# Optimization experiments

Measured on AMD Instinct MI355X. Metric: run time of the kernel, lower is better.

Reference implementation:

```python
import jax, jax.numpy as jnp
import numpy as np

N = 1_000_000
Km = 16
Ks = 64
LB, RT = -1.0, 1.0  # hemi=False -> lb=(-1,-1), rt=(1,1)
TWO_PI = 2.0 * np.pi


def setup_inputs() -> dict:
    key = jax.random.key(0)
    ks = jax.random.split(key, 12)
    r = jax.random.uniform(ks[0], (N, 1), jnp.float32, -0.999, 0.999)
    z = jax.random.uniform(ks[1], (N, 1), jnp.float32, 0.0, TWO_PI)
    theta_w = jax.random.normal(ks[2], (1, Ks), jnp.float32)
    theta_h = jax.random.normal(ks[3], (1, Ks), jnp.float32)
    theta_d = jax.random.normal(ks[4], (1, Ks - 1), jnp.float32)
    W1 = jax.random.normal(ks[5], (1, 64), jnp.float32)
    b1 = jax.random.normal(ks[6], (64,), jnp.float32) * 0.1
    W2 = jax.random.normal(ks[7], (64, 64), jnp.float32) / np.float32(np.sqrt(64))
    b2 = jax.random.normal(ks[8], (64,), jnp.float32) * 0.1
    W3 = jax.random.normal(ks[9], (64, 3 * Km), jnp.float32) / np.float32(np.sqrt(64))
    b3 = jax.random.normal(ks[10], (3 * Km,), jnp.float32) * 0.1
    return dict(r=r, z=z, theta_w=theta_w, theta_h=theta_h, theta_d=theta_d,
                W1=W1, b1=b1, W2=W2, b2=b2, W3=W3, b3=b3)


def _spline(r, theta_w, theta_h, theta_d):
    # Unconditional rational-quadratic circular spline on (LB, RT).
    width = jax.nn.softmax(theta_w, axis=1) * (RT - LB)    # [1,Ks]
    height = jax.nn.softmax(theta_h, axis=1) * (RT - LB)
    zero = jnp.zeros((1, 1), width.dtype)
    x_ks = jnp.concatenate([zero, jnp.cumsum(width, axis=1)], axis=1) + LB   # [1,Ks+1]
    y_ks = jnp.concatenate([zero, jnp.cumsum(height, axis=1)], axis=1) + LB
    bnd = jnp.full((1, 1), (RT - LB) / (RT - LB), width.dtype)
    derivs = jnp.concatenate([bnd, jax.nn.softplus(theta_d) + 0.001, bnd], axis=1)  # [1,Ks+1]

    x = r[:, 0]                                             # [N]
    k = jnp.searchsorted(x_ks[0], x)                        # left side, matches torch default
    k = jnp.where(k == 0, 1, k)
    k = jnp.where(k == Ks + 1, Ks, k)
    k = k - 1
    nk = k + 1
    x_k, x_nk = x_ks[0, k], x_ks[0, nk]
    y_k, y_nk = y_ks[0, k], y_ks[0, nk]
    d_k, d_nk = derivs[0, k], derivs[0, nk]

    s_k = (y_nk - y_k) / (x_nk - x_k)
    eps = (x - x_k) / (x_nk - x_k)
    denom = s_k + (d_nk + d_k - 2.0 * s_k) * eps * (1.0 - eps)
    tx = y_k + (y_nk - y_k) * (s_k * eps ** 2 + d_k * eps * (1.0 - eps)) / denom
    dtx = s_k ** 2 * (d_nk * eps ** 2 + 2.0 * s_k * eps * (1.0 - eps) + d_k * (1.0 - eps) ** 2) / denom ** 2
    return tx[:, None], dtx


def _mobius(x, r, W1, b1, W2, b2, W3, b3):
    # Conditional Mobius transform on the circle; conditioner = 2-hidden MLP on r.
    h = jax.nn.relu(r @ W1 + b1)
    h = jax.nn.relu(h @ W2 + b2)
    theta = h @ W3 + b3                                     # [N,3Km]
    weights = jax.nn.softmax(theta[:, :Km], axis=1)         # [N,Km]
    w = theta[:, Km:].reshape(-1, Km, 2)                    # [N,Km,2]
    w = 0.99 / (1.0 + jnp.linalg.norm(w, axis=-1, keepdims=True)) * w

    def h_map(zv, w):
        # zv: [M,2] broadcast against w: [N,Km,2]
        diff = zv[:, None, :] - w
        wn2 = jnp.sum(w * w, axis=-1, keepdims=True)
        dn2 = jnp.sum(diff * diff, axis=-1, keepdims=True)
        return (1.0 - wn2) / dn2 * diff - w

    zv = jnp.concatenate([jnp.cos(x), jnp.sin(x)], axis=1)  # [N,2]
    h_z = h_map(zv, w)                                      # [N,Km,2]
    h_0 = h_map(jnp.array([[1.0, 0.0]], zv.dtype), w)
    radians = jnp.arctan2(h_z[..., 1], h_z[..., 0])
    shifts = jnp.arctan2(h_0[..., 1], h_0[..., 0])
    tx = radians - shifts
    tx = jnp.where(tx >= 0, tx, tx + TWO_PI)
    t = jnp.sum(weights * tx, axis=1, keepdims=True)        # [N,1]

    # Jacobian magnitude: dh/dz is c*(I - 2 u u^T) (scaled reflection), applied to dz/dtheta
    diff = zv[:, None, :] - w
    dn = jnp.linalg.norm(diff, axis=-1)                     # [N,Km]
    u = diff / dn[..., None]
    dz = jnp.concatenate([-jnp.sin(x), jnp.cos(x)], axis=1) # [N,2]
    c = (1.0 - jnp.sum(w * w, axis=-1)) / dn ** 2           # [N,Km]
    udz = jnp.sum(u * dz[:, None, :], axis=-1)              # [N,Km]
    dh = c[..., None] * (dz[:, None, :] - 2.0 * u * udz[..., None])  # [N,Km,2]
    dt = jnp.sum(jnp.linalg.norm(dh, axis=-1) * weights, axis=1)     # [N]
    return t, dt


def reference(r, z, theta_w, theta_h, theta_d, W1, b1, W2, b2, W3, b3):
    tr, dtr = _spline(r, theta_w, theta_h, theta_d)
    tz, dtz = _mobius(z, r, W1, b1, W2, b2, W3, b3)
    ldj = jnp.log(dtr) + jnp.log(dtz)
    return tr, tz, ldj
```

## Files before the change

### kernel.cpp

```cpp
#include <hip/hip_runtime.h>
#include <math.h>

#define KM 16
#define KS 64
#define TWO_PI_F 6.283185307179586477f

#define WS_SXK   0
#define WS_SYK   65
#define WS_SDK   130
#define WS_KNOT  195
#define WS_A     259
#define WS_B     (259 + 4225)

__device__ __forceinline__ float frcp(float x) { return __builtin_amdgcn_rcpf(x); }

__device__ __forceinline__ float fast_atan2(float y, float x) {
    const float ax = fabsf(x), ay = fabsf(y);
    const float mx = fmaxf(ax, ay), mn = fminf(ax, ay);
    const float t = mn * frcp(mx);
    const float s = t * t;
    float p = -0.01172120f;
    p = fmaf(p, s,  0.05265332f);
    p = fmaf(p, s, -0.11643287f);
    p = fmaf(p, s,  0.19354346f);
    p = fmaf(p, s, -0.33262347f);
    p = fmaf(p, s,  0.99997726f);
    p = p * t;
    p = (ay > ax) ? (1.57079632679f - p) : p;
    p = (x < 0.0f) ? (3.14159265359f - p) : p;
    p = (y < 0.0f) ? -p : p;
    return p;
}

__global__ __launch_bounds__(256)
void precompute_kernel(const float* __restrict__ theta_w,
                       const float* __restrict__ theta_h,
                       const float* __restrict__ theta_d,
                       const float* __restrict__ W1,
                       const float* __restrict__ b1,
                       const float* __restrict__ W2,
                       const float* __restrict__ b2,
                       float* __restrict__ ws)
{
    __shared__ float sW1[64], sb1[64], tjs[64];
    __shared__ int   srnk[64];
    __shared__ float sW2[64 * 64];

    const int tid = threadIdx.x;

    if (tid < 64) {
        const float w1 = W1[tid];
        const float bb = b1[tid];
        sW1[tid] = w1;
        sb1[tid] = bb;
        tjs[tid] = (w1 != 0.0f) ? (-bb / w1) : INFINITY;
    }
    {
        const float4* __restrict__ W2v = (const float4*)W2;
        float4* __restrict__ sW2v = (float4*)sW2;
        for (int t2 = tid; t2 < 1024; t2 += 256) sW2v[t2] = W2v[t2];
    }
    __syncthreads();

    if (tid < 64) {
        const float t = tjs[tid];
        int rk = 0;
        #pragma unroll 1
        for (int k2 = 0; k2 < 64; k2++) {
            const float tk = tjs[k2];
            rk += (tk < t || (tk == t && k2 < tid)) ? 1 : 0;
        }
        srnk[tid] = rk;
    }
    __syncthreads();

    if (blockIdx.x == 0 && tid < 64) {
        ws[WS_KNOT + srnk[tid]] = tjs[tid];

        float vw = theta_w[tid];
        float vh = theta_h[tid];
        float mw = vw, mh = vh;
        #pragma unroll
        for (int off = 32; off > 0; off >>= 1) {
            mw = fmaxf(mw, __shfl_xor(mw, off));
            mh = fmaxf(mh, __shfl_xor(mh, off));
        }
        const float ew = expf(vw - mw);
        const float eh = expf(vh - mh);
        float sumw = ew, sumh = eh;
        #pragma unroll
        for (int off = 32; off > 0; off >>= 1) {
            sumw += __shfl_xor(sumw, off);
            sumh += __shfl_xor(sumh, off);
        }
        float cw = ew / sumw * 2.0f;
        float ch = eh / sumh * 2.0f;
        #pragma unroll
        for (int off = 1; off < 64; off <<= 1) {
            const float uw = __shfl_up(cw, off);
            const float uh = __shfl_up(ch, off);
            if (tid >= off) { cw += uw; ch += uh; }
        }
        ws[WS_SXK + 1 + tid] = cw - 1.0f;
        ws[WS_SYK + 1 + tid] = ch - 1.0f;
        if (tid < KS - 1) {
            const float x = theta_d[tid];
            const float sp = (x > 20.0f) ? x : log1pf(expf(x));
            ws[WS_SDK + 1 + tid] = sp + 0.001f;
        }
        if (tid == 0) {
            ws[WS_SXK] = -1.0f;
            ws[WS_SYK] = -1.0f;
            ws[WS_SDK] = 1.0f;
            ws[WS_SDK + KS] = 1.0f;
        }
    }

    const int p = blockIdx.x * 256 + tid;
    if (p < 65 * 64) {
        const int v = p >> 6;
        const int i = p & 63;
        float cA = 0.0f;
        float cB = b2[i];
        #pragma unroll 1
        for (int j = 0; j < 64; j++) {
            const float w1 = sW1[j];
            const float bb = sb1[j];
            const float w2 = sW2[j * 64 + i];
            if (w1 > 0.0f) {
                if (srnk[j] < v)  { cA = fmaf(w1, w2, cA); cB = fmaf(bb, w2, cB); }
            } else if (w1 < 0.0f) {
                if (srnk[j] >= v) { cA = fmaf(w1, w2, cA); cB = fmaf(bb, w2, cB); }
            } else {
                cB = fmaf(fmaxf(bb, 0.0f), w2, cB);
            }
        }
        ws[WS_A + v * 65 + i] = cA;
        ws[WS_B + v * 65 + i] = cB;
    }
}

__global__ __launch_bounds__(256)
void mobius_spline_kernel(const float* __restrict__ r_in,
                          const float* __restrict__ z_in,
                          const float* __restrict__ W3,
                          const float* __restrict__ b3,
                          const float* __restrict__ ws,
                          float* __restrict__ out,
                          int n)
{
    __shared__ float sxk[KS + 1], syk[KS + 1], sdk[KS + 1];
    __shared__ float sknot[KS];
    __shared__ float sA[65 * 65], sB[65 * 65];

    const int tid = threadIdx.x;

    for (int t2 = tid; t2 < 65; t2 += 256) {
        sxk[t2] = ws[WS_SXK + t2];
        syk[t2] = ws[WS_SYK + t2];
        sdk[t2] = ws[WS_SDK + t2];
    }
    for (int t2 = tid; t2 < 64; t2 += 256) sknot[t2] = ws[WS_KNOT + t2];
    for (int t2 = tid; t2 < 4225; t2 += 256) {
        sA[t2] = ws[WS_A + t2];
        sB[t2] = ws[WS_B + t2];
    }
    __syncthreads();

    const int idx = blockIdx.x * 256 + tid;
    if (idx >= n) return;

    const float rv = r_in[idx];
    const float zz = z_in[idx];

    int lo = 0, hi = KS + 1;
    while (lo < hi) {
        const int mid = (lo + hi) >> 1;
        if (sxk[mid] < rv) lo = mid + 1; else hi = mid;
    }
    int k = lo;
    k = (k == 0) ? 1 : k;
    k = (k == KS + 1) ? KS : k;
    k -= 1;
    const float x_k = sxk[k], x_nk = sxk[k + 1];
    const float y_k = syk[k], y_nk = syk[k + 1];
    const float d_k = sdk[k], d_nk = sdk[k + 1];
    const float rdx = frcp(x_nk - x_k);
    const float dy  = y_nk - y_k;
    const float s_k = dy * rdx;
    const float eps = (rv - x_k) * rdx;
    const float ome = 1.0f - eps;
    const float den = s_k + (d_nk + d_k - 2.0f * s_k) * eps * ome;
    const float rden = frcp(den);
    const float tr  = fmaf(dy * (s_k * eps * eps + d_k * eps * ome), rden, y_k);
    const float dtr = s_k * s_k * (d_nk * eps * eps + 2.0f * s_k * eps * ome + d_k * ome * ome)
                      * rden * rden;

    int lo2 = 0, hi2 = KS;
    while (lo2 < hi2) {
        const int mid = (lo2 + hi2) >> 1;
        if (sknot[mid] < rv) lo2 = mid + 1; else hi2 = mid;
    }
    const int abase = lo2 * 65;

    float th[16], wx[16], wy[16];
    #pragma unroll
    for (int q = 0; q < 16; q++) {
        th[q] = b3[q];
        wx[q] = b3[16 + 2 * q];
        wy[q] = b3[17 + 2 * q];
    }

    #pragma unroll 4
    for (int i = 0; i < 64; i++) {
        const float hv = fmaxf(fmaf(rv, sA[abase + i], sB[abase + i]), 0.0f);
        const float* __restrict__ w3r = &W3[i * 48];
        #pragma unroll
        for (int q = 0; q < 16; q++) {
            th[q] = fmaf(hv, w3r[q],          th[q]);
            wx[q] = fmaf(hv, w3r[16 + 2 * q], wx[q]);
            wy[q] = fmaf(hv, w3r[17 + 2 * q], wy[q]);
        }
    }

    float mx = th[0];
    #pragma unroll
    for (int q = 1; q < 16; q++) mx = fmaxf(mx, th[q]);

    float cz, sz;
    __sincosf(zz, &sz, &cz);

    float wsum = 0.0f, tsum = 0.0f, dsum = 0.0f;

    #pragma unroll
    for (int q = 0; q < 16; q++) {
        const float rwx = wx[q], rwy = wy[q];
        const float nrm = __builtin_amdgcn_sqrtf(rwx * rwx + rwy * rwy);
        const float scl = 0.99f * frcp(1.0f + nrm);
        const float wxx = scl * rwx, wyy = scl * rwy;
        const float wn2 = wxx * wxx + wyy * wyy;
        const float omw = 1.0f - wn2;
        const float dzx = cz - wxx, dzy = sz - wyy;
        const float dn2z = dzx * dzx + dzy * dzy;
        const float cf = omw * frcp(dn2z);
        const float hzx = cf * dzx - wxx;
        const float hzy = cf * dzy - wyy;
        const float d0x = 1.0f - wxx, d0y = -wyy;
        const float dn20 = d0x * d0x + d0y * d0y;
        const float c0 = omw * frcp(dn20);
        const float h0x = c0 * d0x - wxx;
        const float h0y = c0 * d0y - wyy;
        const float cross = hzy * h0x - hzx * h0y;
        const float dotp  = hzx * h0x + hzy * h0y;
        float tx = fast_atan2(cross, dotp);
        tx = (tx >= 0.0f) ? tx : tx + TWO_PI_F;

        const float ew = __expf(th[q] - mx);
        wsum += ew;
        tsum += ew * tx;
        dsum += ew * cf;
    }

    const float inv = frcp(wsum);
    const float tz  = tsum * inv;
    const float dtz = dsum * inv;
    const float ldj = __logf(dtr) + __logf(dtz);

    out[idx]         = tr;
    out[n + idx]     = tz;
    out[2 * n + idx] = ldj;
}

extern "C" void kernel_launch(void* const* d_in, const int* in_sizes, int n_in,
                              void* d_out, int out_size, void* d_ws, size_t ws_size,
                              hipStream_t stream) {
    const int n = in_sizes[0];
    float* ws = (float*)d_ws;

    hipLaunchKernelGGL(precompute_kernel, dim3(17), dim3(256), 0, stream,
                       (const float*)d_in[2], (const float*)d_in[3],
                       (const float*)d_in[4], (const float*)d_in[5],
                       (const float*)d_in[6], (const float*)d_in[7],
                       (const float*)d_in[8], ws);

    const int blocks = (n + 255) / 256;
    hipLaunchKernelGGL(mobius_spline_kernel, dim3(blocks), dim3(256), 0, stream,
                       (const float*)d_in[0], (const float*)d_in[1],
                       (const float*)d_in[9], (const float*)d_in[10],
                       (const float*)ws,
                       (float*)d_out, n);
}
```

Baseline: 179.3 us.

## Precompute piecewise-linear MLP output coefficients per ReLU activation region

The conditioner MLP is piecewise linear in r, so each point's region is set by the layer-1 knot interval and the sorted layer-2 ReLU roots inside it. The new precompute kernel finds those roots for all 65 intervals and precomputes affine coefficients for the 48 outputs in every sub-region. The main kernel then does two small binary searches and evaluates 48 fmas from one global row, replacing the per-point 64x48 layer-3 matmul. The cost is a larger workspace (about 1.6 MB), scattered global reads of the coefficient rows, and a fallback path that runs when the workspace is too small.

Result: faster. 167.4 us (-6.6%).

```diff
diff --git a/kernel.cpp b/kernel.cpp
--- a/kernel.cpp
+++ b/kernel.cpp
@@ -11,6 +11,9 @@
 #define WS_KNOT  195
 #define WS_A     259
 #define WS_B     (259 + 4225)
+#define WS_SROOT 8709
+#define WS_COEF  12872
+#define WS_NEED  (12872 + 4225 * 96)
 
 __device__ __forceinline__ float frcp(float x) { return __builtin_amdgcn_rcpf(x); }
 
@@ -33,35 +36,44 @@
 }
 
 __global__ __launch_bounds__(256)
-void precompute_kernel(const float* __restrict__ theta_w,
-                       const float* __restrict__ theta_h,
-                       const float* __restrict__ theta_d,
-                       const float* __restrict__ W1,
-                       const float* __restrict__ b1,
-                       const float* __restrict__ W2,
-                       const float* __restrict__ b2,
-                       float* __restrict__ ws)
+void precompute_full(const float* __restrict__ theta_w,
+                     const float* __restrict__ theta_h,
+                     const float* __restrict__ theta_d,
+                     const float* __restrict__ W1,
+                     const float* __restrict__ b1,
+                     const float* __restrict__ W2,
+                     const float* __restrict__ b2,
+                     const float* __restrict__ W3,
+                     const float* __restrict__ b3,
+                     float* __restrict__ ws)
 {
-    __shared__ float sW1[64], sb1[64], tjs[64];
+    __shared__ float sW1[64], sb1[64], tjs[64], sknotS[64];
     __shared__ int   srnk[64];
     __shared__ float sW2[64 * 64];
+    __shared__ float sW3[64 * 48];
+    __shared__ float sb3[48];
+    __shared__ float sAv[64], sBv[64], rroot[64], rsort[64], rmid[65];
 
     const int tid = threadIdx.x;
-
-    if (tid < 64) {
-        const float w1 = W1[tid];
-        const float bb = b1[tid];
-        sW1[tid] = w1;
-        sb1[tid] = bb;
-        tjs[tid] = (w1 != 0.0f) ? (-bb / w1) : INFINITY;
-    }
+    const int v = blockIdx.x;
+
+    if (tid < 64) { sW1[tid] = W1[tid]; sb1[tid] = b1[tid]; }
     {
-        const float4* __restrict__ W2v = (const float4*)W2;
-        float4* __restrict__ sW2v = (float4*)sW2;
-        for (int t2 = tid; t2 < 1024; t2 += 256) sW2v[t2] = W2v[t2];
-    }
-    __syncthreads();
-
+        const float4* __restrict__ a = (const float4*)W2;
+        float4* b = (float4*)sW2;
+        for (int t = tid; t < 1024; t += 256) b[t] = a[t];
+    }
+    {
+        const float4* __restrict__ a = (const float4*)W3;
+        float4* b = (float4*)sW3;
+        for (int t = tid; t < 768; t += 256) b[t] = a[t];
+    }
+    if (tid < 48) sb3[tid] = b3[tid];
+    __syncthreads();
+
+    if (tid < 64)
+        tjs[tid] = (sW1[tid] != 0.0f) ? (-sb1[tid] / sW1[tid]) : INFINITY;
+    __syncthreads();
     if (tid < 64) {
         const float t = tjs[tid];
         int rk = 0;
@@ -71,12 +83,289 @@
             rk += (tk < t || (tk == t && k2 < tid)) ? 1 : 0;
         }
         srnk[tid] = rk;
+        sknotS[rk] = t;
+    }
+    __syncthreads();
+
+    if (tid < 64) {
+        const int i = tid;
+        float cA = 0.0f, cB = b2[i];
+        #pragma unroll 1
+        for (int j = 0; j < 64; j++) {
+            const float w1 = sW1[j];
+            const float bb = sb1[j];
+            const float w2 = sW2[j * 64 + i];
+            if (w1 > 0.0f) {
+                if (srnk[j] < v)  { cA = fmaf(w1, w2, cA); cB = fmaf(bb, w2, cB); }
+            } else if (w1 < 0.0f) {
+                if (srnk[j] >= v) { cA = fmaf(w1, w2, cA); cB = fmaf(bb, w2, cB); }
+            } else {
+                cB = fmaf(fmaxf(bb, 0.0f), w2, cB);
+            }
+        }
+        sAv[i] = cA; sBv[i] = cB;
+    }
+    __syncthreads();
+
+    if (tid < 64)
+        rroot[tid] = (sAv[tid] != 0.0f) ? (-sBv[tid] / sAv[tid]) : INFINITY;
+    __syncthreads();
+    if (tid < 64) {
+        const float t = rroot[tid];
+        int rk = 0;
+        #pragma unroll 1
+        for (int k2 = 0; k2 < 64; k2++) {
+            const float tk = rroot[k2];
+            rk += (tk < t || (tk == t && k2 < tid)) ? 1 : 0;
+        }
+        rsort[rk] = t;
+        ws[WS_SROOT + v * 64 + rk] = t;
+    }
+    __syncthreads();
+
+    const float x_lo = (v == 0)  ? -1.0f : sknotS[v - 1];
+    const float x_hi = (v == 64) ?  1.0f : sknotS[v];
+    if (tid < 65) {
+        const int s = tid;
+        const float lo = (s == 0)  ? x_lo : fmaxf(x_lo, rsort[s - 1]);
+        const float hi = (s == 64) ? x_hi : fminf(x_hi, rsort[s]);
+        rmid[s] = 0.5f * (lo + hi);
+    }
+    __syncthreads();
+
+    for (int p = tid; p < 65 * 48; p += 256) {
+        const int s = p / 48;
+        const int o = p - 48 * s;
+        const float rm = rmid[s];
+        float a = 0.0f, b = sb3[o];
+        #pragma unroll 4
+        for (int j = 0; j < 64; j++) {
+            const float A = sAv[j], B = sBv[j];
+            const float w3 = sW3[j * 48 + o];
+            const float m = (fmaf(A, rm, B) > 0.0f) ? w3 : 0.0f;
+            a = fmaf(A, m, a);
+            b = fmaf(B, m, b);
+        }
+        float* __restrict__ row = ws + WS_COEF + (v * 65 + s) * 96;
+        row[2 * o]     = a;
+        row[2 * o + 1] = b;
+    }
+
+    if (v == 0 && tid < 64) {
+        ws[WS_KNOT + tid] = sknotS[tid];
+
+        float vw = theta_w[tid];
+        float vh = theta_h[tid];
+        float mw = vw, mh = vh;
+        #pragma unroll
+        for (int off = 32; off > 0; off >>= 1) {
+            mw = fmaxf(mw, __shfl_xor(mw, off));
+            mh = fmaxf(mh, __shfl_xor(mh, off));
+        }
+        const float ew = expf(vw - mw);
+        const float eh = expf(vh - mh);
+        float sumw = ew, sumh = eh;
+        #pragma unroll
+        for (int off = 32; off > 0; off >>= 1) {
+            sumw += __shfl_xor(sumw, off);
+            sumh += __shfl_xor(sumh, off);
+        }
+        float cw = ew / sumw * 2.0f;
+        float ch = eh / sumh * 2.0f;
+        #pragma unroll
+        for (int off = 1; off < 64; off <<= 1) {
+            const float uw = __shfl_up(cw, off);
+            const float uh = __shfl_up(ch, off);
+            if (tid >= off) { cw += uw; ch += uh; }
+        }
+        ws[WS_SXK + 1 + tid] = cw - 1.0f;
+        ws[WS_SYK + 1 + tid] = ch - 1.0f;
+        if (tid < KS - 1) {
+            const float x = theta_d[tid];
+            const float sp = (x > 20.0f) ? x : log1pf(expf(x));
+            ws[WS_SDK + 1 + tid] = sp + 0.001f;
+        }
+        if (tid == 0) {
+            ws[WS_SXK] = -1.0f;
+            ws[WS_SYK] = -1.0f;
+            ws[WS_SDK] = 1.0f;
+            ws[WS_SDK + KS] = 1.0f;
+        }
+    }
+}
+
+__global__ __launch_bounds__(256)
+void mobius_spline_kernel(const float* __restrict__ r_in,
+                          const float* __restrict__ z_in,
+                          const float* __restrict__ ws,
+                          float* __restrict__ out,
+                          int n)
+{
+    __shared__ float sxk[KS + 1], syk[KS + 1], sdk[KS + 1];
+    __shared__ float sknot[KS];
+    __shared__ float sroots[65 * 65];
+
+    const int tid = threadIdx.x;
+
+    for (int t2 = tid; t2 < 65; t2 += 256) {
+        sxk[t2] = ws[WS_SXK + t2];
+        syk[t2] = ws[WS_SYK + t2];
+        sdk[t2] = ws[WS_SDK + t2];
+    }
+    for (int t2 = tid; t2 < 64; t2 += 256) sknot[t2] = ws[WS_KNOT + t2];
+    for (int t2 = tid; t2 < 65 * 64; t2 += 256) {
+        const int v2 = t2 >> 6, m = t2 & 63;
+        sroots[v2 * 65 + m] = ws[WS_SROOT + t2];
+    }
+    __syncthreads();
+
+    const int idx = blockIdx.x * 256 + tid;
+    if (idx >= n) return;
+
+    const float rv = r_in[idx];
+    const float zz = z_in[idx];
+
+    int lo = 0, hi = KS + 1;
+    while (lo < hi) {
+        const int mid = (lo + hi) >> 1;
+        if (sxk[mid] < rv) lo = mid + 1; else hi = mid;
+    }
+    int k = lo;
+    k = (k == 0) ? 1 : k;
+    k = (k == KS + 1) ? KS : k;
+    k -= 1;
+    const float x_k = sxk[k], x_nk = sxk[k + 1];
+    const float y_k = syk[k], y_nk = syk[k + 1];
+    const float d_k = sdk[k], d_nk = sdk[k + 1];
+    const float rdx = frcp(x_nk - x_k);
+    const float dy  = y_nk - y_k;
+    const float s_k = dy * rdx;
+    const float eps = (rv - x_k) * rdx;
+    const float ome = 1.0f - eps;
+    const float den = s_k + (d_nk + d_k - 2.0f * s_k) * eps * ome;
+    const float rden = frcp(den);
+    const float tr  = fmaf(dy * (s_k * eps * eps + d_k * eps * ome), rden, y_k);
+    const float dtr = s_k * s_k * (d_nk * eps * eps + 2.0f * s_k * eps * ome + d_k * ome * ome)
+                      * rden * rden;
+
+    int lo2 = 0, hi2 = KS;
+    while (lo2 < hi2) {
+        const int mid = (lo2 + hi2) >> 1;
+        if (sknot[mid] < rv) lo2 = mid + 1; else hi2 = mid;
+    }
+    const int v = lo2;
+    const int rbase = v * 65;
+    int lo3 = 0, hi3 = 64;
+    while (lo3 < hi3) {
+        const int mid = (lo3 + hi3) >> 1;
+        if (sroots[rbase + mid] < rv) lo3 = mid + 1; else hi3 = mid;
+    }
+    const int s = lo3;
+
+    const float4* __restrict__ row4 =
+        (const float4*)(ws + WS_COEF + (size_t)(v * 65 + s) * 96);
+
+    float th[16];
+    #pragma unroll
+    for (int o8 = 0; o8 < 8; o8++) {
+        const float4 c = row4[o8];
+        th[2 * o8]     = fmaf(c.x, rv, c.y);
+        th[2 * o8 + 1] = fmaf(c.z, rv, c.w);
+    }
+    float mx = th[0];
+    #pragma unroll
+    for (int q = 1; q < 16; q++) mx = fmaxf(mx, th[q]);
+
+    float cz, sz;
+    __sincosf(zz, &sz, &cz);
+
+    float wsum = 0.0f, tsum = 0.0f, dsum = 0.0f;
+
+    #pragma unroll 4
+    for (int q = 0; q < 16; q++) {
+        const float4 c = row4[8 + q];
+        const float rwx = fmaf(c.x, rv, c.y);
+        const float rwy = fmaf(c.z, rv, c.w);
+        const float nrm = __builtin_amdgcn_sqrtf(rwx * rwx + rwy * rwy);
+        const float scl = 0.99f * frcp(1.0f + nrm);
+        const float wxx = scl * rwx, wyy = scl * rwy;
+        const float wn2 = wxx * wxx + wyy * wyy;
+        const float omw = 1.0f - wn2;
+        const float dzx = cz - wxx, dzy = sz - wyy;
+        const float dn2z = dzx * dzx + dzy * dzy;
+        const float cf = omw * frcp(dn2z);
+        const float hzx = cf * dzx - wxx;
+        const float hzy = cf * dzy - wyy;
+        const float d0x = 1.0f - wxx, d0y = -wyy;
+        const float dn20 = d0x * d0x + d0y * d0y;
+        const float c0 = omw * frcp(dn20);
+        const float h0x = c0 * d0x - wxx;
+        const float h0y = c0 * d0y - wyy;
+        const float cross = hzy * h0x - hzx * h0y;
+        const float dotp  = hzx * h0x + hzy * h0y;
+        float tx = fast_atan2(cross, dotp);
+        tx = (tx >= 0.0f) ? tx : tx + TWO_PI_F;
+
+        const float ew = __expf(th[q] - mx);
+        wsum += ew;
+        tsum += ew * tx;
+        dsum += ew * cf;
+    }
+
+    const float inv = frcp(wsum);
+    const float tz  = tsum * inv;
+    const float dtz = dsum * inv;
+    const float ldj = __logf(dtr) + __logf(dtz);
+
+    out[idx]         = tr;
+    out[n + idx]     = tz;
+    out[2 * n + idx] = ldj;
+}
+
+__global__ __launch_bounds__(256)
+void precompute_fb(const float* __restrict__ theta_w,
+                   const float* __restrict__ theta_h,
+                   const float* __restrict__ theta_d,
+                   const float* __restrict__ W1,
+                   const float* __restrict__ b1,
+                   const float* __restrict__ W2,
+                   const float* __restrict__ b2,
+                   float* __restrict__ ws)
+{
+    __shared__ float sW1[64], sb1[64], tjs[64];
+    __shared__ int   srnk[64];
+    __shared__ float sW2[64 * 64];
+
+    const int tid = threadIdx.x;
+
+    if (tid < 64) {
+        const float w1 = W1[tid];
+        const float bb = b1[tid];
+        sW1[tid] = w1;
+        sb1[tid] = bb;
+        tjs[tid] = (w1 != 0.0f) ? (-bb / w1) : INFINITY;
+    }
+    {
+        const float4* __restrict__ W2v = (const float4*)W2;
+        float4* __restrict__ sW2v = (float4*)sW2;
+        for (int t2 = tid; t2 < 1024; t2 += 256) sW2v[t2] = W2v[t2];
+    }
+    __syncthreads();
+
+    if (tid < 64) {
+        const float t = tjs[tid];
+        int rk = 0;
+        #pragma unroll 1
+        for (int k2 = 0; k2 < 64; k2++) {
+            const float tk = tjs[k2];
+            rk += (tk < t || (tk == t && k2 < tid)) ? 1 : 0;
+        }
+        srnk[tid] = rk;
     }
     __syncthreads();
 
     if (blockIdx.x == 0 && tid < 64) {
         ws[WS_KNOT + srnk[tid]] = tjs[tid];
-
         float vw = theta_w[tid];
         float vh = theta_h[tid];
         float mw = vw, mh = vh;
@@ -141,13 +430,13 @@
 }
 
 __global__ __launch_bounds__(256)
-void mobius_spline_kernel(const float* __restrict__ r_in,
-                          const float* __restrict__ z_in,
-                          const float* __restrict__ W3,
-                          const float* __restrict__ b3,
-                          const float* __restrict__ ws,
-                          float* __restrict__ out,
-                          int n)
+void mobius_spline_fb(const float* __restrict__ r_in,
+                      const float* __restrict__ z_in,
+                      const float* __restrict__ W3,
+                      const float* __restrict__ b3,
+                      const float* __restrict__ ws,
+                      float* __restrict__ out,
+                      int n)
 {
     __shared__ float sxk[KS + 1], syk[KS + 1], sdk[KS + 1];
     __shared__ float sknot[KS];
@@ -276,17 +565,27 @@
                               hipStream_t stream) {
     const int n = in_sizes[0];
     float* ws = (float*)d_ws;
-
-    hipLaunchKernelGGL(precompute_kernel, dim3(17), dim3(256), 0, stream,
-                       (const float*)d_in[2], (const float*)d_in[3],
-                       (const float*)d_in[4], (const float*)d_in[5],
-                       (const float*)d_in[6], (const float*)d_in[7],
-                       (const float*)d_in[8], ws);
-
     const int blocks = (n + 255) / 256;
-    hipLaunchKernelGGL(mobius_spline_kernel, dim3(blocks), dim3(256), 0, stream,
-                       (const float*)d_in[0], (const float*)d_in[1],
-                       (const float*)d_in[9], (const float*)d_in[10],
-                       (const float*)ws,
-                       (float*)d_out, n);
+
+    if (ws_size >= (size_t)WS_NEED * sizeof(float)) {
+        hipLaunchKernelGGL(precompute_full, dim3(65), dim3(256), 0, stream,
+                           (const float*)d_in[2], (const float*)d_in[3],
+                           (const float*)d_in[4], (const float*)d_in[5],
+                           (const float*)d_in[6], (const float*)d_in[7],
+                           (const float*)d_in[8], (const float*)d_in[9],
+                           (const float*)d_in[10], ws);
+        hipLaunchKernelGGL(mobius_spline_kernel, dim3(blocks), dim3(256), 0, stream,
+                           (const float*)d_in[0], (const float*)d_in[1],
+                           (const float*)ws, (float*)d_out, n);
+    } else {
+        hipLaunchKernelGGL(precompute_fb, dim3(17), dim3(256), 0, stream,
+                           (const float*)d_in[2], (const float*)d_in[3],
+                           (const float*)d_in[4], (const float*)d_in[5],
+                           (const float*)d_in[6], (const float*)d_in[7],
+                           (const float*)d_in[8], ws);
+        hipLaunchKernelGGL(mobius_spline_fb, dim3(blocks), dim3(256), 0, stream,
+                           (const float*)d_in[0], (const float*)d_in[1],
+                           (const float*)d_in[9], (const float*)d_in[10],
+                           (const float*)ws, (float*)d_out, n);
+    }
 }
```

## Precompute piecewise-linear layer-3 coefficients per ReLU interval and fuse via cooperative grid

Applied to the files above, without the earlier changes.

Because the input to layer 1 is the scalar r, layers 2 and 3 are piecewise-linear in r. Each of the 65 knot intervals is split again at the 64 layer-2 ReLU roots, and a 48-output affine coefficient pair is precomputed for every sub-interval. Each point then runs two binary searches and reads 96 floats instead of doing a 64x48 matmul. The precompute and main pass are fused into one cooperative persistent kernel with a grid sync, falling back to two launches. The cost is a large coefficient table (about 1.6MB) read from global or L2 per point, with scattered row accesses, and the overhead of the grid sync. Note that the else branch still uses the new layout, so if the workspace is too small the table writes would overflow.

Result: slower. 356.1 us (+98.6%).

```diff
diff --git a/kernel.cpp b/kernel.cpp
--- a/kernel.cpp
+++ b/kernel.cpp
@@ -1,5 +1,8 @@
 #include <hip/hip_runtime.h>
+#include <hip/hip_cooperative_groups.h>
 #include <math.h>
+
+namespace cg = cooperative_groups;
 
 #define KM 16
 #define KS 64
@@ -9,8 +12,9 @@
 #define WS_SYK   65
 #define WS_SDK   130
 #define WS_KNOT  195
-#define WS_A     259
-#define WS_B     (259 + 4225)
+#define WS_SROOT 8709
+#define WS_COEF  12872
+#define WS_NEED  (12872 + 4225 * 96)
 
 __device__ __forceinline__ float frcp(float x) { return __builtin_amdgcn_rcpf(x); }
 
@@ -32,50 +36,101 @@
     return p;
 }
 
-__global__ __launch_bounds__(256)
-void precompute_kernel(const float* __restrict__ theta_w,
-                       const float* __restrict__ theta_h,
-                       const float* __restrict__ theta_d,
-                       const float* __restrict__ W1,
-                       const float* __restrict__ b1,
-                       const float* __restrict__ W2,
-                       const float* __restrict__ b2,
-                       float* __restrict__ ws)
+__device__ __forceinline__ void precompute_interval(
+    int v, int tid,
+    const float* __restrict__ theta_w, const float* __restrict__ theta_h,
+    const float* __restrict__ theta_d,
+    const float* __restrict__ W1, const float* __restrict__ b1,
+    const float* __restrict__ W2, const float* __restrict__ b2,
+    const float* __restrict__ W3, const float* __restrict__ b3,
+    float* __restrict__ ws,
+    float* p_tjs, float* p_sAv, float* p_sBv, float* p_sknotS, float* p_rroot,
+    int* p_srnk, int* p_jinv)
 {
-    __shared__ float sW1[64], sb1[64], tjs[64];
-    __shared__ int   srnk[64];
-    __shared__ float sW2[64 * 64];
-
-    const int tid = threadIdx.x;
-
     if (tid < 64) {
-        const float w1 = W1[tid];
-        const float bb = b1[tid];
-        sW1[tid] = w1;
-        sb1[tid] = bb;
-        tjs[tid] = (w1 != 0.0f) ? (-bb / w1) : INFINITY;
-    }
-    {
-        const float4* __restrict__ W2v = (const float4*)W2;
-        float4* __restrict__ sW2v = (float4*)sW2;
-        for (int t2 = tid; t2 < 1024; t2 += 256) sW2v[t2] = W2v[t2];
-    }
-    __syncthreads();
-
+        const float w1 = W1[tid], bb = b1[tid];
+        p_tjs[tid] = (w1 != 0.0f) ? (-bb / w1) : INFINITY;
+    }
+    __syncthreads();
     if (tid < 64) {
-        const float t = tjs[tid];
+        const float t = p_tjs[tid];
         int rk = 0;
-        #pragma unroll 1
+        #pragma unroll 8
         for (int k2 = 0; k2 < 64; k2++) {
-            const float tk = tjs[k2];
+            const float tk = p_tjs[k2];
             rk += (tk < t || (tk == t && k2 < tid)) ? 1 : 0;
         }
-        srnk[tid] = rk;
-    }
-    __syncthreads();
-
-    if (blockIdx.x == 0 && tid < 64) {
-        ws[WS_KNOT + srnk[tid]] = tjs[tid];
+        p_srnk[tid] = rk;
+        p_sknotS[rk] = t;
+    }
+    __syncthreads();
+
+    if (tid < 64) {
+        const int i = tid;
+        float cA = 0.0f, cB = b2[i];
+        #pragma unroll 8
+        for (int j = 0; j < 64; j++) {
+            const float w1 = W1[j];
+            const float bb = b1[j];
+            const float w2 = W2[j * 64 + i];
+            if (w1 > 0.0f) {
+                if (p_srnk[j] < v)  { cA = fmaf(w1, w2, cA); cB = fmaf(bb, w2, cB); }
+            } else if (w1 < 0.0f) {
+                if (p_srnk[j] >= v) { cA = fmaf(w1, w2, cA); cB = fmaf(bb, w2, cB); }
+            } else {
+                cB = fmaf(fmaxf(bb, 0.0f), w2, cB);
+            }
+        }
+        p_sAv[i] = cA; p_sBv[i] = cB;
+    }
+    __syncthreads();
+
+    if (tid < 64)
+        p_rroot[tid] = (p_sAv[tid] != 0.0f) ? (-p_sBv[tid] / p_sAv[tid]) : INFINITY;
+    __syncthreads();
+    if (tid < 64) {
+        const float t = p_rroot[tid];
+        int rk = 0;
+        #pragma unroll 8
+        for (int k2 = 0; k2 < 64; k2++) {
+            const float tk = p_rroot[k2];
+            rk += (tk < t || (tk == t && k2 < tid)) ? 1 : 0;
+        }
+        p_jinv[rk] = tid;
+        ws[WS_SROOT + v * 64 + rk] = t;
+    }
+    __syncthreads();
+
+    if (tid < 48) {
+        const int o = tid;
+        float a = 0.0f, b = b3[o];
+        #pragma unroll 8
+        for (int j = 0; j < 64; j++) {
+            const float A = p_sAv[j], B = p_sBv[j];
+            const float w3 = W3[j * 48 + o];
+            const bool act = (A < 0.0f) || (A == 0.0f && B > 0.0f);
+            const float m = act ? w3 : 0.0f;
+            a = fmaf(A, m, a);
+            b = fmaf(B, m, b);
+        }
+        float* __restrict__ rowbase = ws + WS_COEF + (size_t)(v * 65) * 96;
+        rowbase[2 * o]     = a;
+        rowbase[2 * o + 1] = b;
+        #pragma unroll 4
+        for (int s = 1; s <= 64; s++) {
+            const int js = p_jinv[s - 1];
+            const float A = p_sAv[js], B = p_sBv[js];
+            const float w3 = W3[js * 48 + o];
+            const float sgn = (A > 0.0f) ? w3 : ((A < 0.0f) ? -w3 : 0.0f);
+            a = fmaf(A, sgn, a);
+            b = fmaf(B, sgn, b);
+            rowbase[s * 96 + 2 * o]     = a;
+            rowbase[s * 96 + 2 * o + 1] = b;
+        }
+    }
+
+    if (v == 0 && tid < 64) {
+        ws[WS_KNOT + tid] = p_sknotS[tid];
 
         float vw = theta_w[tid];
         float vh = theta_h[tid];
@@ -115,64 +170,14 @@
             ws[WS_SDK + KS] = 1.0f;
         }
     }
-
-    const int p = blockIdx.x * 256 + tid;
-    if (p < 65 * 64) {
-        const int v = p >> 6;
-        const int i = p & 63;
-        float cA = 0.0f;
-        float cB = b2[i];
-        #pragma unroll 1
-        for (int j = 0; j < 64; j++) {
-            const float w1 = sW1[j];
-            const float bb = sb1[j];
-            const float w2 = sW2[j * 64 + i];
-            if (w1 > 0.0f) {
-                if (srnk[j] < v)  { cA = fmaf(w1, w2, cA); cB = fmaf(bb, w2, cB); }
-            } else if (w1 < 0.0f) {
-                if (srnk[j] >= v) { cA = fmaf(w1, w2, cA); cB = fmaf(bb, w2, cB); }
-            } else {
-                cB = fmaf(fmaxf(bb, 0.0f), w2, cB);
-            }
-        }
-        ws[WS_A + v * 65 + i] = cA;
-        ws[WS_B + v * 65 + i] = cB;
-    }
-}
-
-__global__ __launch_bounds__(256)
-void mobius_spline_kernel(const float* __restrict__ r_in,
-                          const float* __restrict__ z_in,
-                          const float* __restrict__ W3,
-                          const float* __restrict__ b3,
-                          const float* __restrict__ ws,
-                          float* __restrict__ out,
-                          int n)
+}
+
+__device__ __forceinline__ void main_point(
+    int idx, int n, float rv, float zz,
+    const float* sxk, const float* syk, const float* sdk,
+    const float* sknot, const float* sroots,
+    const float* __restrict__ ws, float* __restrict__ out)
 {
-    __shared__ float sxk[KS + 1], syk[KS + 1], sdk[KS + 1];
-    __shared__ float sknot[KS];
-    __shared__ float sA[65 * 65], sB[65 * 65];
-
-    const int tid = threadIdx.x;
-
-    for (int t2 = tid; t2 < 65; t2 += 256) {
-        sxk[t2] = ws[WS_SXK + t2];
-        syk[t2] = ws[WS_SYK + t2];
-        sdk[t2] = ws[WS_SDK + t2];
-    }
-    for (int t2 = tid; t2 < 64; t2 += 256) sknot[t2] = ws[WS_KNOT + t2];
-    for (int t2 = tid; t2 < 4225; t2 += 256) {
-        sA[t2] = ws[WS_A + t2];
-        sB[t2] = ws[WS_B + t2];
-    }
-    __syncthreads();
-
-    const int idx = blockIdx.x * 256 + tid;
-    if (idx >= n) return;
-
-    const float rv = r_in[idx];
-    const float zz = z_in[idx];
-
     int lo = 0, hi = KS + 1;
     while (lo < hi) {
         const int mid = (lo + hi) >> 1;
@@ -201,28 +206,25 @@
         const int mid = (lo2 + hi2) >> 1;
         if (sknot[mid] < rv) lo2 = mid + 1; else hi2 = mid;
     }
-    const int abase = lo2 * 65;
-
-    float th[16], wx[16], wy[16];
+    const int v = lo2;
+    const int rbase = v * 65;
+    int lo3 = 0, hi3 = 64;
+    while (lo3 < hi3) {
+        const int mid = (lo3 + hi3) >> 1;
+        if (sroots[rbase + mid] < rv) lo3 = mid + 1; else hi3 = mid;
+    }
+    const int s = lo3;
+
+    const float4* __restrict__ row4 =
+        (const float4*)(ws + WS_COEF + (size_t)(v * 65 + s) * 96);
+
+    float th[16];
     #pragma unroll
-    for (int q = 0; q < 16; q++) {
-        th[q] = b3[q];
-        wx[q] = b3[16 + 2 * q];
-        wy[q] = b3[17 + 2 * q];
-    }
-
-    #pragma unroll 4
-    for (int i = 0; i < 64; i++) {
-        const float hv = fmaxf(fmaf(rv, sA[abase + i], sB[abase + i]), 0.0f);
-        const float* __restrict__ w3r = &W3[i * 48];
-        #pragma unroll
-        for (int q = 0; q < 16; q++) {
-            th[q] = fmaf(hv, w3r[q],          th[q]);
-            wx[q] = fmaf(hv, w3r[16 + 2 * q], wx[q]);
-            wy[q] = fmaf(hv, w3r[17 + 2 * q], wy[q]);
-        }
-    }
-
+    for (int o8 = 0; o8 < 8; o8++) {
+        const float4 c = row4[o8];
+        th[2 * o8]     = fmaf(c.x, rv, c.y);
+        th[2 * o8 + 1] = fmaf(c.z, rv, c.w);
+    }
     float mx = th[0];
     #pragma unroll
     for (int q = 1; q < 16; q++) mx = fmaxf(mx, th[q]);
@@ -232,9 +234,11 @@
 
     float wsum = 0.0f, tsum = 0.0f, dsum = 0.0f;
 
-    #pragma unroll
+    #pragma unroll 4
     for (int q = 0; q < 16; q++) {
-        const float rwx = wx[q], rwy = wy[q];
+        const float4 c = row4[8 + q];
+        const float rwx = fmaf(c.x, rv, c.y);
+        const float rwy = fmaf(c.z, rv, c.w);
         const float nrm = __builtin_amdgcn_sqrtf(rwx * rwx + rwy * rwy);
         const float scl = 0.99f * frcp(1.0f + nrm);
         const float wxx = scl * rwx, wyy = scl * rwy;
@@ -271,22 +275,167 @@
     out[2 * n + idx] = ldj;
 }
 
+__global__ __launch_bounds__(256)
+void fused_kernel(const float* __restrict__ r_in,
+                  const float* __restrict__ z_in,
+                  const float* __restrict__ theta_w,
+                  const float* __restrict__ theta_h,
+                  const float* __restrict__ theta_d,
+                  const float* __restrict__ W1,
+                  const float* __restrict__ b1,
+                  const float* __restrict__ W2,
+                  const float* __restrict__ b2,
+                  const float* __restrict__ W3,
+                  const float* __restrict__ b3,
+                  float* __restrict__ ws,
+                  float* __restrict__ out,
+                  int n, int ntiles)
+{
+    __shared__ float sxk[KS + 1], syk[KS + 1], sdk[KS + 1];
+    __shared__ float sknot[KS];
+    __shared__ float sroots[65 * 65];
+    __shared__ float p_tjs[64], p_sAv[64], p_sBv[64], p_sknotS[64], p_rroot[64];
+    __shared__ int   p_srnk[64], p_jinv[64];
+
+    const int tid = threadIdx.x;
+
+    if (blockIdx.x < 65) {
+        precompute_interval(blockIdx.x, tid,
+                            theta_w, theta_h, theta_d, W1, b1, W2, b2, W3, b3,
+                            ws, p_tjs, p_sAv, p_sBv, p_sknotS, p_rroot,
+                            p_srnk, p_jinv);
+    }
+    __threadfence();
+    cg::this_grid().sync();
+    __threadfence();
+
+    for (int t2 = tid; t2 < 65; t2 += 256) {
+        sxk[t2] = ws[WS_SXK + t2];
+        syk[t2] = ws[WS_SYK + t2];
+        sdk[t2] = ws[WS_SDK + t2];
+    }
+    for (int t2 = tid; t2 < 64; t2 += 256) sknot[t2] = ws[WS_KNOT + t2];
+    for (int t2 = tid; t2 < 65 * 64; t2 += 256) {
+        const int v2 = t2 >> 6, m = t2 & 63;
+        sroots[v2 * 65 + m] = ws[WS_SROOT + t2];
+    }
+    __syncthreads();
+
+    for (int tile = blockIdx.x; tile < ntiles; tile += gridDim.x) {
+        const int idx = tile * 256 + tid;
+        if (idx >= n) continue;
+        main_point(idx, n, r_in[idx], z_in[idx],
+                   sxk, syk, sdk, sknot, sroots, ws, out);
+    }
+}
+
+__global__ __launch_bounds__(256)
+void precompute_k(const float* __restrict__ theta_w,
+                  const float* __restrict__ theta_h,
+                  const float* __restrict__ theta_d,
+                  const float* __restrict__ W1,
+                  const float* __restrict__ b1,
+                  const float* __restrict__ W2,
+                  const float* __restrict__ b2,
+                  const float* __restrict__ W3,
+                  const float* __restrict__ b3,
+                  float* __restrict__ ws)
+{
+    __shared__ float p_tjs[64], p_sAv[64], p_sBv[64], p_sknotS[64], p_rroot[64];
+    __shared__ int   p_srnk[64], p_jinv[64];
+    precompute_interval(blockIdx.x, threadIdx.x,
+                        theta_w, theta_h, theta_d, W1, b1, W2, b2, W3, b3,
+                        ws, p_tjs, p_sAv, p_sBv, p_sknotS, p_rroot,
+                        p_srnk, p_jinv);
+}
+
+__global__ __launch_bounds__(256)
+void mobius_spline_kernel(const float* __restrict__ r_in,
+                          const float* __restrict__ z_in,
+                          const float* __restrict__ ws,
+                          float* __restrict__ out,
+                          int n)
+{
+    __shared__ float sxk[KS + 1], syk[KS + 1], sdk[KS + 1];
+    __shared__ float sknot[KS];
+    __shared__ float sroots[65 * 65];
+
+    const int tid = threadIdx.x;
+
+    for (int t2 = tid; t2 < 65; t2 += 256) {
+        sxk[t2] = ws[WS_SXK + t2];
+        syk[t2] = ws[WS_SYK + t2];
+        sdk[t2] = ws[WS_SDK + t2];
+    }
+    for (int t2 = tid; t2 < 64; t2 += 256) sknot[t2] = ws[WS_KNOT + t2];
+    for (int t2 = tid; t2 < 65 * 64; t2 += 256) {
+        const int v2 = t2 >> 6, m = t2 & 63;
+        sroots[v2 * 65 + m] = ws[WS_SROOT + t2];
+    }
+    __syncthreads();
+
+    const int idx = blockIdx.x * 256 + tid;
+    if (idx >= n) return;
+    main_point(idx, n, r_in[idx], z_in[idx],
+               sxk, syk, sdk, sknot, sroots, ws, out);
+}
+
 extern "C" void kernel_launch(void* const* d_in, const int* in_sizes, int n_in,
                               void* d_out, int out_size, void* d_ws, size_t ws_size,
                               hipStream_t stream) {
     const int n = in_sizes[0];
     float* ws = (float*)d_ws;
-
-    hipLaunchKernelGGL(precompute_kernel, dim3(17), dim3(256), 0, stream,
-                       (const float*)d_in[2], (const float*)d_in[3],
-                       (const float*)d_in[4], (const float*)d_in[5],
-                       (const float*)d_in[6], (const float*)d_in[7],
-                       (const float*)d_in[8], ws);
-
-    const int blocks = (n + 255) / 256;
-    hipLaunchKernelGGL(mobius_spline_kernel, dim3(blocks), dim3(256), 0, stream,
-                       (const float*)d_in[0], (const float*)d_in[1],
-                       (const float*)d_in[9], (const float*)d_in[10],
-                       (const float*)ws,
-                       (float*)d_out, n);
-}
+    const int ntiles = (n + 255) / 256;
+
+    const float* r_in = (const float*)d_in[0];
+    const float* z_in = (const float*)d_in[1];
+    const float* tw   = (const float*)d_in[2];
+    const float* thh  = (const float*)d_in[3];
+    const float* td   = (const float*)d_in[4];
+    const float* W1   = (const float*)d_in[5];
+    const float* b1   = (const float*)d_in[6];
+    const float* W2   = (const float*)d_in[7];
+    const float* b2   = (const float*)d_in[8];
+    const float* W3   = (const float*)d_in[9];
+    const float* b3   = (const float*)d_in[10];
+    float* out = (float*)d_out;
+
+    if (ws_size >= (size_t)WS_NEED * sizeof(float)) {
+        static int s_maxGrid = -1;
+        if (s_maxGrid < 0) {
+            int nb = 0, dev = 0, cus = 0;
+            if (hipOccupancyMaxActiveBlocksPerMultiprocessor(&nb, fused_kernel, 256, 0)
+                    == hipSuccess &&
+                hipGetDevice(&dev) == hipSuccess &&
+                hipDeviceGetAttribute(&cus, hipDeviceAttributeMultiprocessorCount, dev)
+                    == hipSuccess && nb > 0 && cus > 0) {
+                s_maxGrid = nb * cus;
+            } else {
+                s_maxGrid = 0;
+            }
+        }
+        int grid = (ntiles < s_maxGrid) ? ntiles : s_maxGrid;
+        if (grid >= 65) {
+            int n_arg = n, nt_arg = ntiles;
+            void* args[] = { (void*)&r_in, (void*)&z_in, (void*)&tw, (void*)&thh,
+                             (void*)&td, (void*)&W1, (void*)&b1, (void*)&W2,
+                             (void*)&b2, (void*)&W3, (void*)&b3, (void*)&ws,
+                             (void*)&out, (void*)&n_arg, (void*)&nt_arg };
+            hipError_t e = hipLaunchCooperativeKernel((const void*)fused_kernel,
+                                                      dim3(grid), dim3(256),
+                                                      args, 0, stream);
+            if (e == hipSuccess) return;
+            (void)hipGetLastError();
+        }
+
+        hipLaunchKernelGGL(precompute_k, dim3(65), dim3(256), 0, stream,
+                           tw, thh, td, W1, b1, W2, b2, W3, b3, ws);
+        hipLaunchKernelGGL(mobius_spline_kernel, dim3(ntiles), dim3(256), 0, stream,
+                           r_in, z_in, ws, out, n);
+    } else {
+        hipLaunchKernelGGL(precompute_k, dim3(65), dim3(256), 0, stream,
+                           tw, thh, td, W1, b1, W2, b2, W3, b3, ws);
+        hipLaunchKernelGGL(mobius_spline_kernel, dim3(ntiles), dim3(256), 0, stream,
+                           r_in, z_in, ws, out, n);
+    }
+}
```
